# Optimization experiments

Hardware: AMD Instinct MI355X
Metric: run time of the kernel (lower is better)

Reference implementation:

```python
import jax, jax.numpy as jnp
import numpy as np

IN_FEATURES = 212445
NODE_SIZES = [IN_FEATURES, 65536, 16384, 128]
N_CLASSES = 20
BATCH = 32


def setup_inputs() -> dict:
    key = jax.random.key(0)
    ks = jax.random.split(key, 16)
    inp = {
        "x": jax.random.normal(ks[0], (BATCH, IN_FEATURES), dtype=jnp.float32),
        "W0": jax.random.normal(ks[1], (32, 1), dtype=jnp.float32) * 0.1,
        "b0": jax.random.normal(ks[2], (32,), dtype=jnp.float32) * 0.1,
        "W1": jax.random.normal(ks[3], (64, 32), dtype=jnp.float32) * 0.1,
        "b1": jax.random.normal(ks[4], (64,), dtype=jnp.float32) * 0.1,
        "W2": jax.random.normal(ks[5], (128, 64), dtype=jnp.float32) * 0.1,
        "b2": jax.random.normal(ks[6], (128,), dtype=jnp.float32) * 0.1,
        "fc_w": jax.random.normal(ks[7], (N_CLASSES, 128 * 128), dtype=jnp.float32) * 0.01,
        "fc_b": jax.random.normal(ks[8], (N_CLASSES,), dtype=jnp.float32) * 0.01,
        # random-tree adjacency: each input node has one parent output node
        "parent0": jax.random.randint(ks[9], (NODE_SIZES[0],), 0, NODE_SIZES[1], dtype=jnp.int32),
        "parent1": jax.random.randint(ks[10], (NODE_SIZES[1],), 0, NODE_SIZES[2], dtype=jnp.int32),
        "parent2": jax.random.randint(ks[11], (NODE_SIZES[2],), 0, NODE_SIZES[3], dtype=jnp.int32),
    }
    return inp


def _fgl(z, parent, n_out, W, b):
    """FGL layer: tree-adjacency reduction over nodes + channel mix.
    z: [N, C_in, n_in] -> [N, C_out, n_out]
    """
    N, C, n_in = z.shape
    # segment-sum reduce input nodes into their parent output node
    zt = jnp.moveaxis(z, 2, 0).reshape(n_in, N * C)          # [n_in, N*C]
    s = jax.ops.segment_sum(zt, parent, num_segments=n_out)  # [n_out, N*C]
    s = jnp.moveaxis(s.reshape(n_out, N, C), 0, 2)           # [N, C_in, n_out]
    # channel mixing (weight-normed linear over channels, shared across nodes)
    return jnp.einsum("oc,ncj->noj", W, s) + b[None, :, None]


def reference(x, W0, b0, W1, b1, W2, b2, fc_w, fc_b, parent0, parent1, parent2):
    N = x.shape[0]
    z = x[:, None, :]                                   # [N, 1, in_features]
    z = _fgl(z, parent0, NODE_SIZES[1], W0, b0)         # [N, 32, 65536]
    z = _fgl(z, parent1, NODE_SIZES[2], W1, b1)         # [N, 64, 16384]
    z = _fgl(z, parent2, NODE_SIZES[3], W2, b2)         # [N, 128, 128]
    logits = z.reshape(N, -1) @ fc_w.T + fc_b           # [N, n_classes]
    return logits
```

## Files before the change

kernel.cpp:

```cpp
#include <hip/hip_runtime.h>

#define IF 212445
#define N1 65536
#define N2 16384
#define NCLS 20
#define BATCH 32
#define HISTB 32
#define MCHUNK 1024
#define MBLK ((IF + MCHUNK - 1) / MCHUNK)
#define TCHUNK 2048
#define NCH ((IF + TCHUNK - 1) / TCHUNK)
#define GRIDM (8 * NCH)

#define OFF_T3   0
#define OFF_HIST 16400
#define OFF_A    49168
#define OFF_SV   59408
#define OFF_SW   69648
#define OFF_CP   79888
#define OFF_MIDX 79968

__global__ __launch_bounds__(256) void k_setup(
    const float* __restrict__ W0, const float* __restrict__ b0,
    const float* __restrict__ W1, const float* __restrict__ b1,
    const float* __restrict__ W2, const float* __restrict__ b2,
    const float* __restrict__ fc_w, const float* __restrict__ fc_b,
    const int* __restrict__ p0, const int* __restrict__ p1,
    const int* __restrict__ p2, char* __restrict__ ws)
{
    int t = threadIdx.x, b = blockIdx.x;
    float* t3   = (float*)(ws + OFF_T3);
    int*   hist = (int*)(ws + OFF_HIST);
    float* A    = (float*)(ws + OFF_A);
    float* Sv   = (float*)(ws + OFF_SV);
    float* Sw   = (float*)(ws + OFF_SW);
    float* CP   = (float*)(ws + OFF_CP);
    int*   midx = (int*)(ws + OFF_MIDX);

    if (b < MBLK) {
        int i = b * MCHUNK + 4 * t;
        if (i + 3 < IF) {
            int4 p = *(const int4*)(p0 + i);
            int4 r;
            r.x = p2[p1[p.x]]; r.y = p2[p1[p.y]];
            r.z = p2[p1[p.z]]; r.w = p2[p1[p.w]];
            *(int4*)(midx + i) = r;
        } else {
            for (int j = i; j < IF; ++j) midx[j] = p2[p1[p0[j]]];
        }
    } else if (b == MBLK) {
        for (int s = t; s < BATCH * 128; s += 256) t3[s] = 0.f;
    } else if (b < MBLK + 1 + HISTB) {
        int hb = b - (MBLK + 1);
        __shared__ int hA[128], hB[128];
        if (t < 128) { hA[t] = 0; hB[t] = 0; }
        __syncthreads();
        const int total = N1 + N2;
        for (int idx = hb * 256 + t; idx < total; idx += HISTB * 256) {
            if (idx < N1) atomicAdd(&hA[p2[p1[idx]]], 1);
            else          atomicAdd(&hB[p2[idx - N1]], 1);
        }
        __syncthreads();
        hist[hb * 256 + t] = (t < 128) ? hA[t] : hB[t - 128];
    } else {
        int cls = b - (MBLK + 1 + HISTB);
        __shared__ float su1[64], sv1[64];
        __shared__ float su2[128], sv2[128], sw2[128], sb2[128];
        __shared__ float pA[256], pV[256], pW[256], pB[256];
        if (t < 64) {
            float a = 0.f, bb = 0.f;
            for (int c = 0; c < 32; ++c) {
                float w = W1[t * 32 + c];
                a += w * W0[c]; bb += w * b0[c];
            }
            su1[t] = a; sv1[t] = bb;
        }
        if (t >= 128) sb2[t - 128] = b2[t - 128];
        __syncthreads();
        if (t < 128) {
            float a = 0.f, bb = 0.f, c = 0.f;
            for (int j = 0; j < 64; ++j) {
                float w = W2[t * 64 + j];
                a += w * su1[j]; bb += w * sv1[j]; c += w * b1[j];
            }
            su2[t] = a; sv2[t] = bb; sw2[t] = c;
        }
        __syncthreads();
        int m = t & 127, h = t >> 7;
        const float* fw = fc_w + cls * 16384 + m;
        float Sa = 0.f, SvA = 0.f, SwA = 0.f, SbA = 0.f;
        #pragma unroll 8
        for (int o = h * 64; o < h * 64 + 64; ++o) {
            float w = fw[o * 128];
            Sa += w * su2[o]; SvA += w * sv2[o];
            SwA += w * sw2[o]; SbA += w * sb2[o];
        }
        pA[t] = Sa; pV[t] = SvA; pW[t] = SwA; pB[t] = SbA;
        __syncthreads();
        if (t < 128) {
            A [cls * 128 + t] = pA[t] + pA[t + 128];
            Sv[cls * 128 + t] = pV[t] + pV[t + 128];
            Sw[cls * 128 + t] = pW[t] + pW[t + 128];
            pB[t] = pB[t] + pB[t + 128];
        }
        __syncthreads();
        for (int s2 = 64; s2 > 0; s2 >>= 1) {
            if (t < s2) pB[t] += pB[t + s2];
            __syncthreads();
        }
        if (t == 0) CP[cls] = fc_b[cls] + pB[0];
    }
}

__global__ __launch_bounds__(256) void k_main(
    const float* __restrict__ x, const int* __restrict__ midx,
    float* __restrict__ t3)
{
    __shared__ float hist[4][512];
    int t = threadIdx.x;
    for (int s = t; s < 2048; s += 256) ((float*)hist)[s] = 0.f;
    __syncthreads();

    int g = blockIdx.x & 7, chunk = blockIdx.x >> 3;
    int r0 = g * 4, base = chunk * TCHUNK;
    const float* x0 = x + (size_t)(r0 + 0) * IF;
    const float* x1 = x + (size_t)(r0 + 1) * IF;
    const float* x2 = x + (size_t)(r0 + 2) * IF;
    const float* x3 = x + (size_t)(r0 + 3) * IF;
    float* hw = &hist[t >> 6][0];

    if (base + TCHUNK <= IF) {
        #pragma unroll 1
        for (int k = 0; k < TCHUNK / 1024; ++k) {
            float v0[4], v1[4], v2[4], v3[4]; int mi[4];
            int i0 = base + k * 1024 + t;
            #pragma unroll
            for (int u = 0; u < 4; ++u) {
                int i = i0 + u * 256;
                mi[u] = midx[i];
                v0[u] = x0[i]; v1[u] = x1[i]; v2[u] = x2[i]; v3[u] = x3[i];
            }
            #pragma unroll
            for (int u = 0; u < 4; ++u) {
                atomicAdd(&hw[      mi[u]], v0[u]);
                atomicAdd(&hw[128 + mi[u]], v1[u]);
                atomicAdd(&hw[256 + mi[u]], v2[u]);
                atomicAdd(&hw[384 + mi[u]], v3[u]);
            }
        }
    } else {
        for (int i = base + t; i < IF; i += 256) {
            int m = midx[i];
            atomicAdd(&hw[      m], x0[i]);
            atomicAdd(&hw[128 + m], x1[i]);
            atomicAdd(&hw[256 + m], x2[i]);
            atomicAdd(&hw[384 + m], x3[i]);
        }
    }
    __syncthreads();
    for (int s = t; s < 512; s += 256) {
        float v = hist[0][s] + hist[1][s] + hist[2][s] + hist[3][s];
        atomicAdd(&t3[(r0 + (s >> 7)) * 128 + (s & 127)], v);
    }
}

__global__ __launch_bounds__(256) void k_epi(
    char* __restrict__ ws, float* __restrict__ out)
{
    __shared__ float smem[7424];
    int t = threadIdx.x;
    const float* t3   = (const float*)(ws + OFF_T3);
    const int*   hist = (const int*)(ws + OFF_HIST);
    const float* A    = (const float*)(ws + OFF_A);
    const float* Svt  = (const float*)(ws + OFF_SV);
    const float* Swt  = (const float*)(ws + OFF_SW);
    const float* CP   = (const float*)(ws + OFF_CP);

    float* st3   = smem;
    float* sA    = smem + 4224;
    float* c2f   = smem + 6784;
    float* cnf   = smem + 6912;
    float* cpart = smem + 7040;
    float* scst  = smem + 7200;

    #pragma unroll
    for (int k = 0; k < 16; ++k) {
        int s = t + 256 * k;
        st3[(s & 127) * 33 + (s >> 7)] = t3[s];
    }
    #pragma unroll
    for (int k = 0; k < 10; ++k) {
        int q = t + 256 * k;
        sA[(q & 127) * 20 + (q >> 7)] = A[q];
    }
    {
        int acc = 0;
        #pragma unroll
        for (int h = 0; h < HISTB; ++h) acc += hist[h * 256 + t];
        if (t < 128) c2f[t] = (float)acc; else cnf[t - 128] = (float)acc;
    }
    __syncthreads();
    if (t < 160) {
        int cls = t >> 3, m0 = (t & 7) * 16;
        const float* sv = Svt + cls * 128;
        const float* sw = Swt + cls * 128;
        float s = 0.f;
        #pragma unroll
        for (int m = m0; m < m0 + 16; ++m)
            s += c2f[m] * sv[m] + cnf[m] * sw[m];
        cpart[t] = s;
    }
    __syncthreads();
    if (t < NCLS) {
        float s = CP[t];
        #pragma unroll
        for (int k = 0; k < 8; ++k) s += cpart[t * 8 + k];
        scst[t] = s;
    }
    __syncthreads();
    #pragma unroll
    for (int k = 0; k < 3; ++k) {
        int p = t + 256 * k;
        if (p < BATCH * NCLS) {
            int n = p / NCLS, cls = p - n * NCLS;
            float acc = scst[cls];
            #pragma unroll 8
            for (int m = 0; m < 128; ++m)
                acc += sA[m * 20 + cls] * st3[m * 33 + n];
            out[p] = acc;
        }
    }
}

extern "C" void kernel_launch(void* const* d_in, const int* in_sizes, int n_in,
                              void* d_out, int out_size, void* d_ws, size_t ws_size,
                              hipStream_t stream)
{
    const float* x    = (const float*)d_in[0];
    const float* W0   = (const float*)d_in[1];
    const float* b0   = (const float*)d_in[2];
    const float* W1   = (const float*)d_in[3];
    const float* b1   = (const float*)d_in[4];
    const float* W2   = (const float*)d_in[5];
    const float* b2   = (const float*)d_in[6];
    const float* fc_w = (const float*)d_in[7];
    const float* fc_b = (const float*)d_in[8];
    const int*   p0   = (const int*)d_in[9];
    const int*   p1   = (const int*)d_in[10];
    const int*   p2   = (const int*)d_in[11];

    char* ws = (char*)d_ws;
    int*  midx = (int*)(ws + OFF_MIDX);
    float* t3  = (float*)(ws + OFF_T3);

    k_setup<<<MBLK + 1 + HISTB + NCLS, 256, 0, stream>>>(
        W0, b0, W1, b1, W2, b2, fc_w, fc_b, p0, p1, p2, ws);
    k_main<<<GRIDM, 256, 0, stream>>>(x, midx, t3);
    k_epi<<<1, 256, 0, stream>>>(ws, (float*)d_out);
}
```

Baseline: 144.0 us.

## Replace global float atomics with per-block partials and a separate reduction kernel

```diff
diff --git a/kernel.cpp b/kernel.cpp
--- a/kernel.cpp
+++ b/kernel.cpp
@@ -19,6 +19,7 @@
 #define OFF_SW   69648
 #define OFF_CP   79888
 #define OFF_MIDX 79968
+#define OFF_PART 929792
 
 __global__ __launch_bounds__(256) void k_setup(
     const float* __restrict__ W0, const float* __restrict__ b0,
@@ -114,11 +115,11 @@
 
 __global__ __launch_bounds__(256) void k_main(
     const float* __restrict__ x, const int* __restrict__ midx,
-    float* __restrict__ t3)
-{
-    __shared__ float hist[4][512];
+    float* __restrict__ part)
+{
+    __shared__ float hist[4][532];
     int t = threadIdx.x;
-    for (int s = t; s < 2048; s += 256) ((float*)hist)[s] = 0.f;
+    for (int s = t; s < 4 * 532; s += 256) ((float*)hist)[s] = 0.f;
     __syncthreads();
 
     int g = blockIdx.x & 7, chunk = blockIdx.x >> 3;
@@ -142,26 +143,42 @@
             }
             #pragma unroll
             for (int u = 0; u < 4; ++u) {
-                atomicAdd(&hw[      mi[u]], v0[u]);
-                atomicAdd(&hw[128 + mi[u]], v1[u]);
-                atomicAdd(&hw[256 + mi[u]], v2[u]);
-                atomicAdd(&hw[384 + mi[u]], v3[u]);
+                unsafeAtomicAdd(&hw[      mi[u]], v0[u]);
+                unsafeAtomicAdd(&hw[132 + mi[u]], v1[u]);
+                unsafeAtomicAdd(&hw[264 + mi[u]], v2[u]);
+                unsafeAtomicAdd(&hw[396 + mi[u]], v3[u]);
             }
         }
     } else {
         for (int i = base + t; i < IF; i += 256) {
             int m = midx[i];
-            atomicAdd(&hw[      m], x0[i]);
-            atomicAdd(&hw[128 + m], x1[i]);
-            atomicAdd(&hw[256 + m], x2[i]);
-            atomicAdd(&hw[384 + m], x3[i]);
-        }
-    }
-    __syncthreads();
+            unsafeAtomicAdd(&hw[      m], x0[i]);
+            unsafeAtomicAdd(&hw[132 + m], x1[i]);
+            unsafeAtomicAdd(&hw[264 + m], x2[i]);
+            unsafeAtomicAdd(&hw[396 + m], x3[i]);
+        }
+    }
+    __syncthreads();
+    float* pb = part + (size_t)blockIdx.x * 512;
     for (int s = t; s < 512; s += 256) {
-        float v = hist[0][s] + hist[1][s] + hist[2][s] + hist[3][s];
-        atomicAdd(&t3[(r0 + (s >> 7)) * 128 + (s & 127)], v);
-    }
+        int r = s >> 7, m = s & 127;
+        int o = r * 132 + m;
+        pb[s] = hist[0][o] + hist[1][o] + hist[2][o] + hist[3][o];
+    }
+}
+
+__global__ __launch_bounds__(256) void k_red(
+    const float* __restrict__ part, float* __restrict__ t3)
+{
+    int tid = blockIdx.x * 256 + threadIdx.x;
+    int row = tid >> 7, m = tid & 127;
+    int g = row >> 2, r = row & 3;
+    const float* p = part + (size_t)g * 512 + r * 128 + m;
+    float s = 0.f;
+    #pragma unroll 8
+    for (int c = 0; c < NCH; ++c)
+        s += p[(size_t)c * 8 * 512];
+    t3[row * 128 + m] = s;
 }
 
 __global__ __launch_bounds__(256) void k_epi(
@@ -250,11 +267,13 @@
     const int*   p2   = (const int*)d_in[11];
 
     char* ws = (char*)d_ws;
-    int*  midx = (int*)(ws + OFF_MIDX);
-    float* t3  = (float*)(ws + OFF_T3);
+    int*   midx = (int*)(ws + OFF_MIDX);
+    float* t3   = (float*)(ws + OFF_T3);
+    float* part = (float*)(ws + OFF_PART);
 
     k_setup<<<MBLK + 1 + HISTB + NCLS, 256, 0, stream>>>(
         W0, b0, W1, b1, W2, b2, fc_w, fc_b, p0, p1, p2, ws);
-    k_main<<<GRIDM, 256, 0, stream>>>(x, midx, t3);
+    k_main<<<GRIDM, 256, 0, stream>>>(x, midx, part);
+    k_red<<<16, 256, 0, stream>>>(part, t3);
     k_epi<<<1, 256, 0, stream>>>(ws, (float*)d_out);
 }
```

Measured after the change: 148.2 us. 1.03x slower.
